# Kernel tuning notes

Measured on AMD Instinct MI355X. Metric: run time of the kernel, lower is better.

The kernel has to match this reference:

```python
import jax, jax.numpy as jnp
import numpy as np

LAMBDA_TEMP = 20.0
GAMMA = 20.0
MARGIN = 0.05
EPS = 1e-8

B, K, M, D = 128, 256, 8, 128


def _unit(x, axis=-1):
    return x / jnp.linalg.norm(x, axis=axis, keepdims=True)


def setup_inputs() -> dict:
    key = jax.random.key(0)
    k1, k2, k3 = jax.random.split(key, 3)
    v_proj = _unit(jax.random.normal(k1, (B, K, D), dtype=jnp.float32))
    prototypes = _unit(jax.random.normal(k2, (K, M, D), dtype=jnp.float32))
    concept_labels = jax.random.randint(k3, (B, K), 0, 2, dtype=jnp.int64)
    return {"v_proj": v_proj, "concept_labels": concept_labels, "prototypes": prototypes}


def reference(v_proj, concept_labels, prototypes):
    # all-pairs prototype similarities: query vector (b,k) vs prototypes of concept c
    # sims: (B, K, C, M)
    sims = jnp.einsum('bkd,cmd->bkcm', v_proj, prototypes)
    # Eq.6: soft assignment over the M prototypes of each concept
    q = jax.nn.softmax(GAMMA * sims, axis=-1)
    # Eq.7-8: weighted similarity sim_c(v)  -> (B, K, C)
    sim = jnp.sum(q * sims, axis=-1)
    # positive similarity: concept k queried against its own prototypes, plus margin
    sim_pos = jnp.einsum('bkk->bk', sim) + MARGIN  # (B, K)
    # Eq.9: -log( exp(lam*sim_pos) / (sum_c exp(lam*sim_c) + eps) )
    denom = jnp.sum(jnp.exp(LAMBDA_TEMP * sim), axis=-1) + EPS  # (B, K)
    loss_bk = jnp.log(denom) - LAMBDA_TEMP * sim_pos  # (B, K)
    mask = (concept_labels == 1).astype(loss_bk.dtype)
    num_pos = jnp.sum(mask)
    total = jnp.sum(loss_bk * mask)
    return jnp.where(num_pos > 0, total / num_pos, total)
```

## Files before the change

kernel.cpp:

```cpp
#include <hip/hip_runtime.h>

#define LT      20.0f
#define LN2     0.69314718055994531f
#define C2EXP   28.853900817779268f
#define CHUNKS  16
#define NBLK    512

typedef _Float16 half8  __attribute__((ext_vector_type(8)));
typedef float    f32x16 __attribute__((ext_vector_type(16)));

#if __has_builtin(__builtin_amdgcn_exp2f)
#define EXP2F(x) __builtin_amdgcn_exp2f(x)
#else
#define EXP2F(x) __expf(0.69314718055994531f * (x))
#endif

#define GLD16(gp, lp) __builtin_amdgcn_global_load_lds( \
    (const __attribute__((address_space(1))) void*)(gp), \
    (__attribute__((address_space(3))) void*)(lp), 16, 0, 0)


__global__ __launch_bounds__(1024)
void mpcl_prep_compact(const float* __restrict__ P,
                       const int*   __restrict__ labels,
                       _Float16* __restrict__ Pw,
                       int* __restrict__ ridx, int* __restrict__ npos)
{
    __shared__ int wcnt[512];
    __shared__ int wsum[8];
    __shared__ int sbase[512];
    __shared__ int tot;

    if (blockIdx.x < 32) {
        int t    = blockIdx.x * 1024 + threadIdx.x;
        int gcol = t >> 4;
        int dblk = t & 15;
        const float* src = P + ((size_t)gcol << 7) + dblk * 8;
        float4 x0 = *(const float4*)src;
        float4 x1 = *(const float4*)(src + 4);

        int ch = gcol >> 7, col = gcol & 127;
        int g  = col >> 5,  col5 = col & 31;
        int cl = col5 >> 3, p = col5 & 7;
        int a  = (p & 3) | ((cl & 1) << 2) | ((cl >> 1) << 3) | ((p >> 2) << 4);
        int hi = dblk & 1, s = dblk >> 1;
        int l  = (hi << 5) | a;
        int slot = ch * 2048 + (g * 8 + s) * 64 + l;

        half8 hv;
        hv[0] = (_Float16)(C2EXP * x0.x); hv[1] = (_Float16)(C2EXP * x0.y);
        hv[2] = (_Float16)(C2EXP * x0.z); hv[3] = (_Float16)(C2EXP * x0.w);
        hv[4] = (_Float16)(C2EXP * x1.x); hv[5] = (_Float16)(C2EXP * x1.y);
        hv[6] = (_Float16)(C2EXP * x1.z); hv[7] = (_Float16)(C2EXP * x1.w);
        *(half8*)(Pw + (size_t)slot * 8) = hv;
    } else {
        const int tid = threadIdx.x, lane = tid & 63, w = tid >> 6;
        int lab[32];
#pragma unroll
        for (int i = 0; i < 32; ++i) lab[i] = labels[i * 1024 + tid];
#pragma unroll
        for (int i = 0; i < 32; ++i) {
            unsigned long long m = __ballot(lab[i] == 1);
            if (lane == 0) wcnt[i * 16 + w] = __popcll(m);
        }
        __syncthreads();

        int v = 0, orig = 0;
        if (tid < 512) { v = wcnt[tid]; orig = v; }
#pragma unroll
        for (int off = 1; off < 64; off <<= 1) {
            int t2 = __shfl_up(v, off);
            if (lane >= off) v += t2;
        }
        if (lane == 63 && w < 8) wsum[w] = v;
        __syncthreads();
        if (tid == 0) {
            int acc = 0;
#pragma unroll
            for (int i = 0; i < 8; ++i) { int t2 = wsum[i]; wsum[i] = acc; acc += t2; }
            tot = acc; npos[0] = acc;
        }
        __syncthreads();
        if (tid < 512) sbase[tid] = v - orig + wsum[w];
        __syncthreads();

#pragma unroll
        for (int i = 0; i < 32; ++i) {
            unsigned long long m = __ballot(lab[i] == 1);
            int pos = sbase[i * 16 + w] + __popcll(m & ((1ull << lane) - 1));
            if (lab[i] == 1) ridx[pos] = i * 1024 + tid;
        }
        for (int j = tot + tid; j < 32768; j += 1024) ridx[j] = 0;
    }
}

__global__ __attribute__((amdgpu_flat_work_group_size(512, 512),
                          amdgpu_waves_per_eu(2, 2)))
void mpcl_main(const float* __restrict__ V,
               const _Float16* __restrict__ Pw,
               const int* __restrict__ ridx,
               const int* __restrict__ npos,
               float* __restrict__ part)
{
    __shared__ __align__(16) _Float16 Pst[8 * 4096];
    __shared__ float sh_denom[64];
    __shared__ float sh_simpos[64];

    const int np = *npos;
    const int rowbase = blockIdx.x * 64;
    if (rowbase >= np) return;

    const int tid = threadIdx.x;
    const int l   = tid & 63;
    const int w   = tid >> 6;
    const int g   = w & 3;
    const int kh  = w >> 2;
    const int a   = l & 31;
    const int hi  = l >> 5;

    if (tid < 64) { sh_denom[tid] = 0.0f; sh_simpos[tid] = 0.0f; }

    int myrow[2], rowk[2];
    half8 vh[2][8];
#pragma unroll
    for (int rf = 0; rf < 2; ++rf) {
        int pos = rowbase + rf * 32 + a;
        myrow[rf] = ridx[pos < np ? pos : np - 1];
        rowk[rf]  = myrow[rf] & 255;
        const float* vr = V + ((size_t)myrow[rf] << 7) + hi * 8;
#pragma unroll
        for (int s = 0; s < 8; ++s) {
            float4 x0 = *(const float4*)(vr + s * 16);
            float4 x1 = *(const float4*)(vr + s * 16 + 4);
            vh[rf][s][0] = (_Float16)x0.x; vh[rf][s][1] = (_Float16)x0.y;
            vh[rf][s][2] = (_Float16)x0.z; vh[rf][s][3] = (_Float16)x0.w;
            vh[rf][s][4] = (_Float16)x1.x; vh[rf][s][5] = (_Float16)x1.y;
            vh[rf][s][6] = (_Float16)x1.z; vh[rf][s][7] = (_Float16)x1.w;
        }
    }
    __syncthreads();

    const _Float16* gbase = Pw + (size_t)g * 4096 + (size_t)l * 8;
    _Float16* lbase = &Pst[w * 4096];

#define STAGEH(CH, HF, B) do {                                        \
    const _Float16* g_ = gbase + (size_t)(CH) * 16384 + (HF) * 2048;  \
    _Float16* l_ = lbase + (B) * 2048;                                \
    GLD16(g_,        l_);        GLD16(g_ +  512, l_ +  512);         \
    GLD16(g_ + 1024, l_ + 1024); GLD16(g_ + 1536, l_ + 1536);         \
} while (0)

    const int ch0 = kh * 8;
    STAGEH(ch0, 0, 0);
    STAGEH(ch0, 1, 1);

    float dn0 = 0.f, dn1 = 0.f;

#define SOFT8(y0,y1,y2,y3,y4,y5,y6,y7, CONCEPT, DN, SLOT) do {              \
    float e0=EXP2F(y0), e1=EXP2F(y1), e2=EXP2F(y2), e3=EXP2F(y3);           \
    float e4=EXP2F(y4), e5=EXP2F(y5), e6=EXP2F(y6), e7=EXP2F(y7);           \
    float es = ((e0+e1)+(e2+e3)) + ((e4+e5)+(e6+e7));                       \
    float ss = fmaf(e0,y0, fmaf(e1,y1, fmaf(e2,y2, e3*y3)))                 \
             + fmaf(e4,y4, fmaf(e5,y5, fmaf(e6,y6, e7*y7)));                \
    float simY = __fdividef(ss, es);                   \
    DN += EXP2F(simY);                                                      \
    if ((CONCEPT) == rowk[(SLOT) >> 5]) sh_simpos[SLOT] = simY;             \
} while (0)

#pragma unroll 1
    for (int i = 0; i < 8; ++i) {
        const int ch = ch0 + i;

        f32x16 ac0 = {0.f,0.f,0.f,0.f,0.f,0.f,0.f,0.f,0.f,0.f,0.f,0.f,0.f,0.f,0.f,0.f};
        f32x16 ac1 = {0.f,0.f,0.f,0.f,0.f,0.f,0.f,0.f,0.f,0.f,0.f,0.f,0.f,0.f,0.f,0.f};

        asm volatile("s_waitcnt vmcnt(4)" ::: "memory");
        {
            const _Float16* bs = lbase;
            half8 p0 = *(const half8*)&bs[l * 8];
            half8 p1 = *(const half8*)&bs[l * 8 + 512];
            half8 p2 = *(const half8*)&bs[l * 8 + 1024];
            half8 p3 = *(const half8*)&bs[l * 8 + 1536];
            ac0 = __builtin_amdgcn_mfma_f32_32x32x16_f16(p0, vh[0][0], ac0, 0, 0, 0);
            ac1 = __builtin_amdgcn_mfma_f32_32x32x16_f16(p0, vh[1][0], ac1, 0, 0, 0);
            ac0 = __builtin_amdgcn_mfma_f32_32x32x16_f16(p1, vh[0][1], ac0, 0, 0, 0);
            ac1 = __builtin_amdgcn_mfma_f32_32x32x16_f16(p1, vh[1][1], ac1, 0, 0, 0);
            ac0 = __builtin_amdgcn_mfma_f32_32x32x16_f16(p2, vh[0][2], ac0, 0, 0, 0);
            ac1 = __builtin_amdgcn_mfma_f32_32x32x16_f16(p2, vh[1][2], ac1, 0, 0, 0);
            ac0 = __builtin_amdgcn_mfma_f32_32x32x16_f16(p3, vh[0][3], ac0, 0, 0, 0);
            ac1 = __builtin_amdgcn_mfma_f32_32x32x16_f16(p3, vh[1][3], ac1, 0, 0, 0);
        }
        asm volatile("s_waitcnt lgkmcnt(0)" ::: "memory");
        if (i + 1 < 8) STAGEH(ch + 1, 0, 0);

        if (i < 7) asm volatile("s_waitcnt vmcnt(4)" ::: "memory");
        else       asm volatile("s_waitcnt vmcnt(0)" ::: "memory");
        {
            const _Float16* bs = lbase + 2048;
            half8 p4 = *(const half8*)&bs[l * 8];
            half8 p5 = *(const half8*)&bs[l * 8 + 512];
            half8 p6 = *(const half8*)&bs[l * 8 + 1024];
            half8 p7 = *(const half8*)&bs[l * 8 + 1536];
            ac0 = __builtin_amdgcn_mfma_f32_32x32x16_f16(p4, vh[0][4], ac0, 0, 0, 0);
            ac1 = __builtin_amdgcn_mfma_f32_32x32x16_f16(p4, vh[1][4], ac1, 0, 0, 0);
            ac0 = __builtin_amdgcn_mfma_f32_32x32x16_f16(p5, vh[0][5], ac0, 0, 0, 0);
            ac1 = __builtin_amdgcn_mfma_f32_32x32x16_f16(p5, vh[1][5], ac1, 0, 0, 0);
            ac0 = __builtin_amdgcn_mfma_f32_32x32x16_f16(p6, vh[0][6], ac0, 0, 0, 0);
            ac1 = __builtin_amdgcn_mfma_f32_32x32x16_f16(p6, vh[1][6], ac1, 0, 0, 0);
            ac0 = __builtin_amdgcn_mfma_f32_32x32x16_f16(p7, vh[0][7], ac0, 0, 0, 0);
            ac1 = __builtin_amdgcn_mfma_f32_32x32x16_f16(p7, vh[1][7], ac1, 0, 0, 0);
        }
        asm volatile("s_waitcnt lgkmcnt(0)" ::: "memory");
        if (i + 1 < 8) STAGEH(ch + 1, 1, 1);

        const int cb = (ch << 4) + (g << 2) + hi;
        SOFT8(ac0[0], ac0[1], ac0[2],  ac0[3],  ac0[8],  ac0[9],  ac0[10], ac0[11], cb,     dn0, a);
        SOFT8(ac0[4], ac0[5], ac0[6],  ac0[7],  ac0[12], ac0[13], ac0[14], ac0[15], cb + 2, dn0, a);
        SOFT8(ac1[0], ac1[1], ac1[2],  ac1[3],  ac1[8],  ac1[9],  ac1[10], ac1[11], cb,     dn1, 32 + a);
        SOFT8(ac1[4], ac1[5], ac1[6],  ac1[7],  ac1[12], ac1[13], ac1[14], ac1[15], cb + 2, dn1, 32 + a);
    }

    {
        float t0 = dn0 + __shfl_xor(dn0, 32);
        float t1 = dn1 + __shfl_xor(dn1, 32);
        if (hi == 0) {
            atomicAdd(&sh_denom[a],      t0);
            atomicAdd(&sh_denom[32 + a], t1);
        }
    }
    __syncthreads();

    if (w == 0) {
        float s = 0.f, cc = 0.f;
        if (rowbase + l < np) {
            s  = logf(sh_denom[l] + 1e-8f) - LN2 * sh_simpos[l] - 1.0f;
            cc = 1.0f;
        }
#pragma unroll
        for (int off = 32; off >= 1; off >>= 1) {
            s  += __shfl_down(s, off);
            cc += __shfl_down(cc, off);
        }
        if (l == 0) {
            part[2 * blockIdx.x]     = s;
            part[2 * blockIdx.x + 1] = cc;
        }
    }
}

__global__ __launch_bounds__(512)
void mpcl_finish(const float* __restrict__ part, const int* __restrict__ npos,
                 float* __restrict__ out)
{
    __shared__ float sh[16];
    const int tid  = threadIdx.x;
    const int lane = tid & 63;
    const int w    = tid >> 6;
    const int nact = (*npos + 63) >> 6;

    float s = 0.f, cc = 0.f;
    for (int i = tid; i < nact; i += 512) {
        s  += part[2 * i];
        cc += part[2 * i + 1];
    }
#pragma unroll
    for (int off = 32; off >= 1; off >>= 1) {
        s  += __shfl_down(s, off);
        cc += __shfl_down(cc, off);
    }
    if (lane == 0) { sh[w] = s; sh[8 + w] = cc; }
    __syncthreads();
    if (tid == 0) {
        float ts = 0.f, tc = 0.f;
#pragma unroll
        for (int i = 0; i < 8; ++i) { ts += sh[i]; tc += sh[8 + i]; }
        out[0] = (tc > 0.0f) ? (ts / tc) : ts;
    }
}

extern "C" void kernel_launch(void* const* d_in, const int* in_sizes, int n_in,
                              void* d_out, int out_size, void* d_ws, size_t ws_size,
                              hipStream_t stream)
{
    const float* V      = (const float*)d_in[0];
    const int*   labels = (const int*)d_in[1];
    const float* P      = (const float*)d_in[2];
    float* out = (float*)d_out;

    int*      npos = (int*)d_ws;
    float*    part = (float*)((char*)d_ws + 256);
    int*      ridx = (int*)((char*)d_ws + 16384);
    _Float16* Pw   = (_Float16*)((char*)d_ws + 147456);

    mpcl_prep_compact<<<33, 1024, 0, stream>>>(P, labels, Pw, ridx, npos);
    mpcl_main<<<NBLK, 512, 0, stream>>>(V, Pw, ridx, npos, part);
    mpcl_finish<<<1, 512, 0, stream>>>(part, npos, out);
}
```

Baseline: 93.56 us.

## Load prototypes directly into registers and replicate Pw across eight copies

The main kernel no longer stages prototype tiles through LDS with global_load_lds. Each wave now loads its half8 fragments straight from global memory into registers, double-buffered across chunks and ordered with sched_barrier. The prep kernel writes eight replicated copies of the converted prototype buffer, and each block reads the copy picked by blockIdx&7, to spread L2/channel contention. This adds register pressure (16 half8 buffers), a larger prep kernel (257 blocks), and 4 MB of workspace writes.

```diff
diff --git a/kernel.cpp b/kernel.cpp
--- a/kernel.cpp
+++ b/kernel.cpp
@@ -5,6 +5,7 @@
 #define C2EXP   28.853900817779268f
 #define CHUNKS  16
 #define NBLK    512
+#define PW_COPY 262144
 
 typedef _Float16 half8  __attribute__((ext_vector_type(8)));
 typedef float    f32x16 __attribute__((ext_vector_type(16)));
@@ -15,10 +16,6 @@
 #define EXP2F(x) __expf(0.69314718055994531f * (x))
 #endif
 
-#define GLD16(gp, lp) __builtin_amdgcn_global_load_lds( \
-    (const __attribute__((address_space(1))) void*)(gp), \
-    (__attribute__((address_space(3))) void*)(lp), 16, 0, 0)
-
 
 __global__ __launch_bounds__(1024)
 void mpcl_prep_compact(const float* __restrict__ P,
@@ -31,8 +28,9 @@
     __shared__ int sbase[512];
     __shared__ int tot;
 
-    if (blockIdx.x < 32) {
-        int t    = blockIdx.x * 1024 + threadIdx.x;
+    if (blockIdx.x < 256) {
+        int copy = blockIdx.x & 7;
+        int t    = (blockIdx.x >> 3) * 1024 + threadIdx.x;
         int gcol = t >> 4;
         int dblk = t & 15;
         const float* src = P + ((size_t)gcol << 7) + dblk * 8;
@@ -52,7 +50,7 @@
         hv[2] = (_Float16)(C2EXP * x0.z); hv[3] = (_Float16)(C2EXP * x0.w);
         hv[4] = (_Float16)(C2EXP * x1.x); hv[5] = (_Float16)(C2EXP * x1.y);
         hv[6] = (_Float16)(C2EXP * x1.z); hv[7] = (_Float16)(C2EXP * x1.w);
-        *(half8*)(Pw + (size_t)slot * 8) = hv;
+        *(half8*)(Pw + (size_t)copy * PW_COPY + (size_t)slot * 8) = hv;
     } else {
         const int tid = threadIdx.x, lane = tid & 63, w = tid >> 6;
         int lab[32];
@@ -102,7 +100,6 @@
                const int* __restrict__ npos,
                float* __restrict__ part)
 {
-    __shared__ __align__(16) _Float16 Pst[8 * 4096];
     __shared__ float sh_denom[64];
     __shared__ float sh_simpos[64];
 
@@ -140,21 +137,14 @@
     }
     __syncthreads();
 
-    const _Float16* gbase = Pw + (size_t)g * 4096 + (size_t)l * 8;
-    _Float16* lbase = &Pst[w * 4096];
-
-#define STAGEH(CH, HF, B) do {                                        \
-    const _Float16* g_ = gbase + (size_t)(CH) * 16384 + (HF) * 2048;  \
-    _Float16* l_ = lbase + (B) * 2048;                                \
-    GLD16(g_,        l_);        GLD16(g_ +  512, l_ +  512);         \
-    GLD16(g_ + 1024, l_ + 1024); GLD16(g_ + 1536, l_ + 1536);         \
+    const half8* pw = (const half8*)(Pw + (size_t)(blockIdx.x & 7) * PW_COPY)
+                    + (size_t)g * 512 + l;
+
+#define LOADCH(CH, BUF) do {                                   \
+    _Pragma("unroll")                                          \
+    for (int s = 0; s < 8; ++s)                                \
+        BUF[s] = pw[(size_t)(CH) * 2048 + s * 64];             \
 } while (0)
-
-    const int ch0 = kh * 8;
-    STAGEH(ch0, 0, 0);
-    STAGEH(ch0, 1, 1);
-
-    float dn0 = 0.f, dn1 = 0.f;
 
 #define SOFT8(y0,y1,y2,y3,y4,y5,y6,y7, CONCEPT, DN, SLOT) do {              \
     float e0=EXP2F(y0), e1=EXP2F(y1), e2=EXP2F(y2), e3=EXP2F(y3);           \
@@ -167,57 +157,36 @@
     if ((CONCEPT) == rowk[(SLOT) >> 5]) sh_simpos[SLOT] = simY;             \
 } while (0)
 
+#define COMPUTE(BUF, CH) do {                                               \
+    f32x16 ac0 = {0.f,0.f,0.f,0.f,0.f,0.f,0.f,0.f,0.f,0.f,0.f,0.f,0.f,0.f,0.f,0.f}; \
+    f32x16 ac1 = {0.f,0.f,0.f,0.f,0.f,0.f,0.f,0.f,0.f,0.f,0.f,0.f,0.f,0.f,0.f,0.f}; \
+    _Pragma("unroll")                                                       \
+    for (int s = 0; s < 8; ++s) {                                           \
+        ac0 = __builtin_amdgcn_mfma_f32_32x32x16_f16(BUF[s], vh[0][s], ac0, 0, 0, 0); \
+        ac1 = __builtin_amdgcn_mfma_f32_32x32x16_f16(BUF[s], vh[1][s], ac1, 0, 0, 0); \
+    }                                                                       \
+    const int cb = ((CH) << 4) + (g << 2) + hi;     \
+    SOFT8(ac0[0], ac0[1], ac0[2],  ac0[3],  ac0[8],  ac0[9],  ac0[10], ac0[11], cb,     dn0, a); \
+    SOFT8(ac0[4], ac0[5], ac0[6],  ac0[7],  ac0[12], ac0[13], ac0[14], ac0[15], cb + 2, dn0, a); \
+    SOFT8(ac1[0], ac1[1], ac1[2],  ac1[3],  ac1[8],  ac1[9],  ac1[10], ac1[11], cb,     dn1, 32 + a); \
+    SOFT8(ac1[4], ac1[5], ac1[6],  ac1[7],  ac1[12], ac1[13], ac1[14], ac1[15], cb + 2, dn1, 32 + a); \
+} while (0)
+
+    float dn0 = 0.f, dn1 = 0.f;
+    const int ch0 = kh * 8;
+
+    half8 pA[8], pB[8];
+    LOADCH(ch0, pA);
+
 #pragma unroll 1
-    for (int i = 0; i < 8; ++i) {
-        const int ch = ch0 + i;
-
-        f32x16 ac0 = {0.f,0.f,0.f,0.f,0.f,0.f,0.f,0.f,0.f,0.f,0.f,0.f,0.f,0.f,0.f,0.f};
-        f32x16 ac1 = {0.f,0.f,0.f,0.f,0.f,0.f,0.f,0.f,0.f,0.f,0.f,0.f,0.f,0.f,0.f,0.f};
-
-        asm volatile("s_waitcnt vmcnt(4)" ::: "memory");
-        {
-            const _Float16* bs = lbase;
-            half8 p0 = *(const half8*)&bs[l * 8];
-            half8 p1 = *(const half8*)&bs[l * 8 + 512];
-            half8 p2 = *(const half8*)&bs[l * 8 + 1024];
-            half8 p3 = *(const half8*)&bs[l * 8 + 1536];
-            ac0 = __builtin_amdgcn_mfma_f32_32x32x16_f16(p0, vh[0][0], ac0, 0, 0, 0);
-            ac1 = __builtin_amdgcn_mfma_f32_32x32x16_f16(p0, vh[1][0], ac1, 0, 0, 0);
-            ac0 = __builtin_amdgcn_mfma_f32_32x32x16_f16(p1, vh[0][1], ac0, 0, 0, 0);
-            ac1 = __builtin_amdgcn_mfma_f32_32x32x16_f16(p1, vh[1][1], ac1, 0, 0, 0);
-            ac0 = __builtin_amdgcn_mfma_f32_32x32x16_f16(p2, vh[0][2], ac0, 0, 0, 0);
-            ac1 = __builtin_amdgcn_mfma_f32_32x32x16_f16(p2, vh[1][2], ac1, 0, 0, 0);
-            ac0 = __builtin_amdgcn_mfma_f32_32x32x16_f16(p3, vh[0][3], ac0, 0, 0, 0);
-            ac1 = __builtin_amdgcn_mfma_f32_32x32x16_f16(p3, vh[1][3], ac1, 0, 0, 0);
-        }
-        asm volatile("s_waitcnt lgkmcnt(0)" ::: "memory");
-        if (i + 1 < 8) STAGEH(ch + 1, 0, 0);
-
-        if (i < 7) asm volatile("s_waitcnt vmcnt(4)" ::: "memory");
-        else       asm volatile("s_waitcnt vmcnt(0)" ::: "memory");
-        {
-            const _Float16* bs = lbase + 2048;
-            half8 p4 = *(const half8*)&bs[l * 8];
-            half8 p5 = *(const half8*)&bs[l * 8 + 512];
-            half8 p6 = *(const half8*)&bs[l * 8 + 1024];
-            half8 p7 = *(const half8*)&bs[l * 8 + 1536];
-            ac0 = __builtin_amdgcn_mfma_f32_32x32x16_f16(p4, vh[0][4], ac0, 0, 0, 0);
-            ac1 = __builtin_amdgcn_mfma_f32_32x32x16_f16(p4, vh[1][4], ac1, 0, 0, 0);
-            ac0 = __builtin_amdgcn_mfma_f32_32x32x16_f16(p5, vh[0][5], ac0, 0, 0, 0);
-            ac1 = __builtin_amdgcn_mfma_f32_32x32x16_f16(p5, vh[1][5], ac1, 0, 0, 0);
-            ac0 = __builtin_amdgcn_mfma_f32_32x32x16_f16(p6, vh[0][6], ac0, 0, 0, 0);
-            ac1 = __builtin_amdgcn_mfma_f32_32x32x16_f16(p6, vh[1][6], ac1, 0, 0, 0);
-            ac0 = __builtin_amdgcn_mfma_f32_32x32x16_f16(p7, vh[0][7], ac0, 0, 0, 0);
-            ac1 = __builtin_amdgcn_mfma_f32_32x32x16_f16(p7, vh[1][7], ac1, 0, 0, 0);
-        }
-        asm volatile("s_waitcnt lgkmcnt(0)" ::: "memory");
-        if (i + 1 < 8) STAGEH(ch + 1, 1, 1);
-
-        const int cb = (ch << 4) + (g << 2) + hi;
-        SOFT8(ac0[0], ac0[1], ac0[2],  ac0[3],  ac0[8],  ac0[9],  ac0[10], ac0[11], cb,     dn0, a);
-        SOFT8(ac0[4], ac0[5], ac0[6],  ac0[7],  ac0[12], ac0[13], ac0[14], ac0[15], cb + 2, dn0, a);
-        SOFT8(ac1[0], ac1[1], ac1[2],  ac1[3],  ac1[8],  ac1[9],  ac1[10], ac1[11], cb,     dn1, 32 + a);
-        SOFT8(ac1[4], ac1[5], ac1[6],  ac1[7],  ac1[12], ac1[13], ac1[14], ac1[15], cb + 2, dn1, 32 + a);
+    for (int i = 0; i < 8; i += 2) {
+        LOADCH(ch0 + i + 1, pB);
+        __builtin_amdgcn_sched_barrier(0);
+        COMPUTE(pA, ch0 + i);
+
+        if (i + 2 < 8) LOADCH(ch0 + i + 2, pA);
+        __builtin_amdgcn_sched_barrier(0);
+        COMPUTE(pB, ch0 + i + 1);
     }
 
     {
@@ -292,7 +261,7 @@
     int*      ridx = (int*)((char*)d_ws + 16384);
     _Float16* Pw   = (_Float16*)((char*)d_ws + 147456);
 
-    mpcl_prep_compact<<<33, 1024, 0, stream>>>(P, labels, Pw, ridx, npos);
+    mpcl_prep_compact<<<257, 1024, 0, stream>>>(P, labels, Pw, ridx, npos);
     mpcl_main<<<NBLK, 512, 0, stream>>>(V, Pw, ridx, npos, part);
     mpcl_finish<<<1, 512, 0, stream>>>(part, npos, out);
 }
```

Result: no change. 93.73 us (+0.2%).
